# Kernel tuning notes

Hardware: AMD Instinct MI355X
Metric: run time of the kernel (lower is better)

The kernel has to match this reference:

```python
import jax, jax.numpy as jnp
import numpy as np

V = 50257  # vocab_size
H = 512    # d_model
S = 512    # source length
B = 8      # batch
T = 64     # decode steps


def setup_inputs() -> dict:
    key = jax.random.key(0)
    k1, k2, k3, k4, k5, k6 = jax.random.split(key, 6)
    src_full = jax.random.randint(k1, (S, B), 0, V, dtype=jnp.int32)
    decode_output = jax.random.normal(k2, (T, B, H), dtype=jnp.float32)
    decode_attn = jax.random.uniform(k3, (B, T, S), dtype=jnp.float32)
    memory = jax.random.normal(k4, (S, B, H), dtype=jnp.float32)
    # learned params: gen_proj (H->V) and prob_proj (H->1)
    W_gen = jax.random.normal(k5, (H, V), dtype=jnp.float32) / np.sqrt(H)
    b_gen = jnp.zeros((V,), dtype=jnp.float32)
    W_prob = jax.random.normal(k6, (H, 1), dtype=jnp.float32) / np.sqrt(H)
    b_prob = jnp.zeros((1,), dtype=jnp.float32)
    return {
        "src_full": src_full,
        "decode_output": decode_output,
        "decode_attn": decode_attn,
        "memory": memory,
        "W_gen": W_gen,
        "b_gen": b_gen,
        "W_prob": W_prob,
        "b_prob": b_prob,
    }


def reference(src_full, decode_output, decode_attn, memory, W_gen, b_gen, W_prob, b_prob):
    # context[t,b,h] = sum_s attn[b,t,s] * memory[s,b,h]
    context = jnp.einsum("bts,sbh->tbh", decode_attn, memory)  # [T,B,H]
    prob = jax.nn.sigmoid(context @ W_prob + b_prob)           # [T,B,1] copy gate p_gen
    gen_logits = prob * jax.nn.softmax(decode_output @ W_gen + b_gen, axis=-1)  # [T,B,V]

    # scatter-add attention mass onto vocab slots: copy[t,b, src_full[s,b]] += attn[b,t,s]
    attn_tbs = jnp.transpose(decode_attn, (1, 0, 2))  # [T,B,S]
    idx = src_full.T                                  # [B,S]
    ti = jnp.arange(T)[:, None, None]
    bi = jnp.arange(B)[None, :, None]
    copy_logits = jnp.zeros((T, B, V), dtype=decode_attn.dtype).at[ti, bi, idx[None, :, :]].add(attn_tbs)
    copy_logits = (1.0 - prob) * jax.nn.softmax(copy_logits, axis=-1)

    return jnp.log(gen_logits + copy_logits)
```

## Files before the change

### kernel.cpp

```cpp
#include <hip/hip_runtime.h>
#include <hip/hip_bf16.h>
#include <math.h>

#define VV 50257
#define VP 50304
#define HH 512
#define SS 512
#define BB 8
#define TT 64
#define MM (TT*BB)

typedef __bf16 bf16x2 __attribute__((ext_vector_type(2)));
typedef __bf16 bf16x4 __attribute__((ext_vector_type(4)));
typedef __bf16 bf16x8 __attribute__((ext_vector_type(8)));
typedef float  f32x4  __attribute__((ext_vector_type(4)));

__device__ __forceinline__ __bf16 f2b(float f) {
    unsigned u = __builtin_bit_cast(unsigned, f);
    unsigned r = (u + 0x7fffu + ((u >> 16) & 1u)) >> 16;
    unsigned short s = (unsigned short)r;
    return __builtin_bit_cast(__bf16, s);
}

__device__ __forceinline__ void gl2lds16(const void* g, void* l) {
    __builtin_amdgcn_global_load_lds(
        (const __attribute__((address_space(1))) unsigned*)g,
        (__attribute__((address_space(3))) unsigned*)l, 16, 0, 0);
}

__global__ __launch_bounds__(256) void k_castA(const float* __restrict__ A,
                                               __bf16* __restrict__ Ab) {
    int i = (blockIdx.x * 256 + threadIdx.x) * 4;
    float4 v = *(const float4*)&A[i];
    bf16x4 o = {f2b(v.x), f2b(v.y), f2b(v.z), f2b(v.w)};
    *(bf16x4*)&Ab[i] = o;
}

__global__ __launch_bounds__(256) void k_castWT(const float* __restrict__ W,
                                                __bf16* __restrict__ Wt) {
    __shared__ float tile[64][65];
    int n0 = blockIdx.x * 64;
    int k0 = blockIdx.y * 64;
    int tid = threadIdx.x;
#pragma unroll
    for (int i = 0; i < 16; i++) {
        int idx = tid + i * 256;
        int kk = idx >> 6, nn = idx & 63;
        int n = n0 + nn;
        tile[kk][nn] = (n < VV) ? W[(size_t)(k0 + kk) * VV + n] : 0.f;
    }
    __syncthreads();
#pragma unroll
    for (int i = 0; i < 8; i++) {
        int idx = tid + i * 256;
        int nn = idx >> 5, kp = idx & 31;
        bf16x2 o = {f2b(tile[2 * kp][nn]), f2b(tile[2 * kp + 1][nn])};
        *(bf16x2*)&Wt[(size_t)(n0 + nn) * HH + k0 + 2 * kp] = o;
    }
}

__global__ void k_mw(const float* __restrict__ mem, const float* __restrict__ Wp,
                     float* __restrict__ mw) {
    int row = blockIdx.x;
    int lane = threadIdx.x;
    const float* mp = mem + (size_t)row * HH;
    float acc = 0.f;
#pragma unroll
    for (int i = 0; i < HH / 64; i++)
        acc += mp[lane + 64 * i] * Wp[lane + 64 * i];
#pragma unroll
    for (int off = 32; off > 0; off >>= 1) acc += __shfl_down(acc, off);
    if (lane == 0) mw[row] = acc;
}

__global__ void k_prob(const float* __restrict__ attn, const float* __restrict__ mw,
                       const float* __restrict__ bp, float* __restrict__ prob) {
    int r = blockIdx.x;
    int t = r / BB, b = r % BB;
    int lane = threadIdx.x;
    const float* ap = attn + ((size_t)b * TT + t) * SS;
    float acc = 0.f;
#pragma unroll
    for (int i = 0; i < SS / 64; i++) {
        int s = lane + 64 * i;
        acc += ap[s] * mw[s * BB + b];
    }
#pragma unroll
    for (int off = 32; off > 0; off >>= 1) acc += __shfl_down(acc, off);
    if (lane == 0) prob[r] = 1.f / (1.f + expf(-(acc + bp[0])));
}

template<bool BF16OUT>
__global__ __launch_bounds__(512, 4) void k_gemm3(const __bf16* __restrict__ Ab,
                                                  const __bf16* __restrict__ Wt,
                                                  const float* __restrict__ bias,
                                                  float* __restrict__ Cf,
                                                  __bf16* __restrict__ Cb,
                                                  float* __restrict__ Zrow) {
    __shared__ __bf16 As[2][8192];
    __shared__ __bf16 Bs[2][8192];
    __shared__ float zred[128];

    const int tid  = threadIdx.x;
    const int lane = tid & 63;
    const int wave = tid >> 6;
    const int l15  = lane & 15;
    const int quad = lane >> 4;
    const int wr = (wave >> 2) * 64;
    const int wc = (wave & 3) * 32;

    int L = blockIdx.x + gridDim.x * blockIdx.y;
    int xcd = L & 7, i8 = L >> 3;
    int nid = (xcd < 4 ? xcd * 197 : 4 * 197 + (xcd - 4) * 196) + i8;
    const int row0 = (nid & 3) * 128;
    const int col0 = (nid >> 2) * 128;

    size_t offA[2], offB[2];
#pragma unroll
    for (int j = 0; j < 2; j++) {
        offA[j] = (size_t)(row0 + wave * 16 + l15) * HH + (j * 4 + quad) * 8;
        offB[j] = (size_t)(col0 + wave * 16 + l15) * HH + (j * 4 + quad) * 8;
    }

#define STAGE(buf, k0)                                                    \
    do {                                                                  \
        _Pragma("unroll") for (int j = 0; j < 2; j++) {                   \
            gl2lds16(Ab + offA[j] + (k0), &As[buf][wave * 1024 + j * 512]); \
            gl2lds16(Wt + offB[j] + (k0), &Bs[buf][wave * 1024 + j * 512]); \
        }                                                                 \
    } while (0)

    f32x4 acc[4][2] = {};

    STAGE(0, 0);
    for (int it = 0; it < 8; ++it) {
        __syncthreads();
        if (it != 7) STAGE((it + 1) & 1, (it + 1) * 64);
        const __bf16* Al = &As[it & 1][0];
        const __bf16* Bl = &Bs[it & 1][0];
#pragma unroll
        for (int h = 0; h < 2; ++h) {
            bf16x8 af[4], bfv[2];
#pragma unroll
            for (int mt = 0; mt < 4; mt++)
                af[mt] = *(const bf16x8*)&Al[((wr >> 4) + mt) * 1024 + h * 512 + lane * 8];
#pragma unroll
            for (int nt = 0; nt < 2; nt++)
                bfv[nt] = *(const bf16x8*)&Bl[((wc >> 4) + nt) * 1024 + h * 512 + lane * 8];
#pragma unroll
            for (int mt = 0; mt < 4; mt++)
#pragma unroll
                for (int nt = 0; nt < 2; nt++)
                    acc[mt][nt] = __builtin_amdgcn_mfma_f32_16x16x32_bf16(
                        af[mt], bfv[nt], acc[mt][nt], 0, 0, 0);
        }
    }
#undef STAGE

    __syncthreads();
    if (tid < 128) zred[tid] = 0.f;
    __syncthreads();

#pragma unroll
    for (int mt = 0; mt < 4; mt++) {
        float esum[4] = {0.f, 0.f, 0.f, 0.f};
#pragma unroll
        for (int nt = 0; nt < 2; nt++) {
            int c = col0 + wc + nt * 16 + l15;
            if (c < VV) {
                float bv = bias[c];
#pragma unroll
                for (int i = 0; i < 4; i++) {
                    int r = row0 + wr + mt * 16 + quad * 4 + i;
                    float l = acc[mt][nt][i] + bv;
                    if (BF16OUT) Cb[(size_t)r * VP + c] = f2b(l);
                    else         Cf[(size_t)r * VV + c] = l;
                    esum[i] += __expf(l);
                }
            }
        }
#pragma unroll
        for (int i = 0; i < 4; i++) {
            float e = esum[i];
            e += __shfl_xor(e, 1);
            e += __shfl_xor(e, 2);
            e += __shfl_xor(e, 4);
            e += __shfl_xor(e, 8);
            if (l15 == 0)
                atomicAdd(&zred[wr + mt * 16 + quad * 4 + i], e);
        }
    }
    __syncthreads();
    if (tid < 128) atomicAdd(&Zrow[row0 + tid], zred[tid]);
}

#define HT 1024
#define NBW 1572

__device__ __forceinline__ void build_hash(const int* __restrict__ src,
                                           const float* __restrict__ ap,
                                           int b, int tid,
                                           int* keys, float* vals, unsigned* bmap,
                                           float* red, int* s_D, float* s_Zc) {
    for (int i = tid; i < HT; i += 256) { keys[i] = -1; vals[i] = 0.f; }
    for (int i = tid; i < NBW; i += 256) bmap[i] = 0u;
    if (tid == 0) *s_D = 0;
    __syncthreads();

    for (int s = tid; s < SS; s += 256) {
        int idx = src[s * BB + b];
        float v = ap[s];
        unsigned h = ((unsigned)idx * 2654435761u) >> 22;
        while (true) {
            int old = atomicCAS(&keys[h], -1, idx);
            if (old == -1 || old == idx) { atomicAdd(&vals[h], v); break; }
            h = (h + 1) & (HT - 1);
        }
    }
    __syncthreads();

    float lsum = 0.f; int dloc = 0;
    for (int i = tid; i < HT; i += 256) {
        int k = keys[i];
        if (k != -1) {
            lsum += __expf(vals[i]); dloc++;
            atomicOr(&bmap[(unsigned)k >> 5], 1u << (k & 31));
        }
    }
    atomicAdd(s_D, dloc);
    red[tid] = lsum; __syncthreads();
    for (int st = 128; st > 0; st >>= 1) {
        if (tid < st) red[tid] += red[tid + st];
        __syncthreads();
    }
    if (tid == 0) *s_Zc = (float)(VV - *s_D) + red[0];
    __syncthreads();
}

__global__ __launch_bounds__(1024) void k_final_row(const int* __restrict__ src,
                                                    const float* __restrict__ attn,
                                                    const float* __restrict__ prob,
                                                    const float* __restrict__ Zrow,
                                                    const __bf16* __restrict__ LG,
                                                    float* __restrict__ out) {
    __shared__ int      keys[HT];
    __shared__ float    vals[HT];
    __shared__ unsigned bmap[NBW];
    __shared__ float    red[1024];
    __shared__ int      s_D;
    __shared__ float    s_Zc;

    int r = blockIdx.x;
    int t = r / BB, b = r % BB;
    int tid = threadIdx.x;
    const float* ap = attn + ((size_t)b * TT + t) * SS;

    { int i = tid; keys[i] = -1; vals[i] = 0.f; }
    for (int i = tid; i < NBW; i += 1024) bmap[i] = 0u;
    if (tid == 0) s_D = 0;
    __syncthreads();

    if (tid < SS) {
        int idx = src[tid * BB + b];
        float v = ap[tid];
        unsigned h = ((unsigned)idx * 2654435761u) >> 22;
        while (true) {
            int old = atomicCAS(&keys[h], -1, idx);
            if (old == -1 || old == idx) { atomicAdd(&vals[h], v); break; }
            h = (h + 1) & (HT - 1);
        }
    }
    __syncthreads();

    float lsum = 0.f;
    {
        int k = keys[tid];
        bool occ = (k != -1);
        if (occ) {
            lsum = __expf(vals[tid]);
            atomicOr(&bmap[(unsigned)k >> 5], 1u << (k & 31));
        }
        unsigned long long m = __ballot(occ);
        if ((tid & 63) == 0) atomicAdd(&s_D, __popcll(m));
    }
    red[tid] = lsum; __syncthreads();
    for (int st = 512; st > 0; st >>= 1) {
        if (tid < st) red[tid] += red[tid + st];
        __syncthreads();
    }
    if (tid == 0) s_Zc = (float)(VV - s_D) + red[0];
    __syncthreads();

    float p = prob[r];
    float pinvZ = p / Zrow[r];
    float qinvZc = (1.f - p) / s_Zc;

    const __bf16* lrow = LG + (size_t)r * VP;
    float* orow = out + (size_t)r * VV;

    for (int v0 = tid * 8; v0 < VP; v0 += 8192) {
        bf16x8 l8 = *(const bf16x8*)&lrow[v0];
#pragma unroll
        for (int e = 0; e < 8; e++) {
            int v = v0 + e;
            if (v < VV) {
                float l = (float)l8[e];
                float c = 1.f;
                if ((bmap[v >> 5] >> (v & 31)) & 1u) {
                    unsigned h = ((unsigned)v * 2654435761u) >> 22;
                    while (true) {
                        int k = keys[h];
                        if (k == v) { c = __expf(vals[h]); break; }
                        if (k == -1) break;
                        h = (h + 1) & (HT - 1);
                    }
                }
                orow[v] = __logf(pinvZ * __expf(l) + qinvZc * c);
            }
        }
    }
}

#define CHUNKS 6283
__global__ __launch_bounds__(256) void k_final_s(const int* __restrict__ src,
                                                 const float* __restrict__ attn,
                                                 const float* __restrict__ prob,
                                                 const float* __restrict__ Zrow,
                                                 float* __restrict__ out) {
    __shared__ int      keys[HT];
    __shared__ float    vals[HT];
    __shared__ unsigned bmap[NBW];
    __shared__ float    red[256];
    __shared__ int      s_D;
    __shared__ float    s_Zc;

    int r = blockIdx.y;
    int t = r / BB, b = r % BB;
    int tid = threadIdx.x;
    const float* ap = attn + ((size_t)b * TT + t) * SS;
    build_hash(src, ap, b, tid, keys, vals, bmap, red, &s_D, &s_Zc);

    float p = prob[r];
    float pinvZ = p / Zrow[r];
    float qinvZc = (1.f - p) / s_Zc;

    int c0 = blockIdx.x * CHUNKS;
    int c1 = c0 + CHUNKS; if (c1 > VV) c1 = VV;
    float* rowp = out + (size_t)r * VV;

    for (int v = c0 + tid; v < c1; v += 256) {
        float l = rowp[v];
        float c = 1.f;
        if ((bmap[v >> 5] >> (v & 31)) & 1u) {
            unsigned h = ((unsigned)v * 2654435761u) >> 22;
            while (true) {
                int k = keys[h];
                if (k == v) { c = __expf(vals[h]); break; }
                if (k == -1) break;
                h = (h + 1) & (HT - 1);
            }
        }
        rowp[v] = __logf(pinvZ * __expf(l) + qinvZc * c);
    }
}

extern "C" void kernel_launch(void* const* d_in, const int* in_sizes, int n_in,
                              void* d_out, int out_size, void* d_ws, size_t ws_size,
                              hipStream_t stream) {
    const int*   src_full      = (const int*)d_in[0];
    const float* decode_output = (const float*)d_in[1];
    const float* decode_attn   = (const float*)d_in[2];
    const float* memory        = (const float*)d_in[3];
    const float* W_gen         = (const float*)d_in[4];
    const float* b_gen         = (const float*)d_in[5];
    const float* W_prob        = (const float*)d_in[6];
    const float* b_prob        = (const float*)d_in[7];
    float* out = (float*)d_out;

    float* ws   = (float*)d_ws;
    float* mw   = ws;
    float* prob = ws + 4096;
    float* Z    = ws + 4608;
    __bf16* Ab  = (__bf16*)(ws + 5120);
    __bf16* Wt  = (__bf16*)(ws + 5120 + 131072);
    __bf16* LG  = Wt + (size_t)VP * HH;

    size_t base_b = (size_t)(5120 + 131072) * sizeof(float);
    size_t wt_b   = (size_t)VP * HH * 2;
    size_t lg_b   = (size_t)MM * VP * 2;
    bool full = ws_size >= base_b + wt_b + lg_b;

    k_castA<<<MM * HH / (256 * 4), 256, 0, stream>>>(decode_output, Ab);
    k_mw<<<SS * BB, 64, 0, stream>>>(memory, W_prob, mw);
    k_prob<<<TT * BB, 64, 0, stream>>>(decode_attn, mw, b_prob, prob);
    hipMemsetAsync(Z, 0, MM * sizeof(float), stream);

    dim3 tgrid(VP / 64, HH / 64);
    k_castWT<<<tgrid, 256, 0, stream>>>(W_gen, Wt);

    dim3 ggrid(MM / 128, VP / 128);
    if (full) {
        k_gemm3<true><<<ggrid, 512, 0, stream>>>(Ab, Wt, b_gen, nullptr, LG, Z);
        k_final_row<<<MM, 1024, 0, stream>>>(src_full, decode_attn, prob, Z, LG, out);
    } else {
        k_gemm3<false><<<ggrid, 512, 0, stream>>>(Ab, Wt, b_gen, out, nullptr, Z);
        dim3 fgrid((VV + CHUNKS - 1) / CHUNKS, MM);
        k_final_s<<<fgrid, 256, 0, stream>>>(src_full, decode_attn, prob, Z, out);
    }
}
```

Measured before the change: 364.8 us.

## Merge preprocessing launches and deepen GEMM LDS pipeline to four stages

The small preprocessing kernels (A cast, memory·W_prob dot, prob gate, Z memset, W transpose-cast) are merged into two combined launches, with Z zeroed inside the prob blocks instead of by a memset. The GEMM's K loop changes from double-buffered 64-wide steps to a four-buffer, 32-wide ring. Each step uses explicit vmcnt waits and a raw barrier, so up to three stages of global-to-LDS loads are in flight at once. This is meant to cut launch overhead and hide load latency, at the cost of more loop iterations and hand-managed wait counts that must match the issued loads exactly.

Result: faster. 355.3 us (-2.6%).

```diff
diff --git a/kernel.cpp b/kernel.cpp
--- a/kernel.cpp
+++ b/kernel.cpp
@@ -28,77 +28,90 @@
         (__attribute__((address_space(3))) unsigned*)l, 16, 0, 0);
 }
 
-__global__ __launch_bounds__(256) void k_castA(const float* __restrict__ A,
-                                               __bf16* __restrict__ Ab) {
-    int i = (blockIdx.x * 256 + threadIdx.x) * 4;
-    float4 v = *(const float4*)&A[i];
-    bf16x4 o = {f2b(v.x), f2b(v.y), f2b(v.z), f2b(v.w)};
-    *(bf16x4*)&Ab[i] = o;
-}
-
-__global__ __launch_bounds__(256) void k_castWT(const float* __restrict__ W,
-                                                __bf16* __restrict__ Wt) {
+#define WAITV(n) asm volatile("s_waitcnt vmcnt(" #n ")" ::: "memory")
+
+__global__ __launch_bounds__(256) void k_pre(const float* __restrict__ A,
+                                             __bf16* __restrict__ Ab,
+                                             const float* __restrict__ mem,
+                                             const float* __restrict__ Wp,
+                                             float* __restrict__ mw) {
+    int tid = threadIdx.x;
+    if (blockIdx.x < 256) {
+        int i = (blockIdx.x * 256 + tid) * 4;
+        float4 v = *(const float4*)&A[i];
+        bf16x4 o = {f2b(v.x), f2b(v.y), f2b(v.z), f2b(v.w)};
+        *(bf16x4*)&Ab[i] = o;
+    } else {
+        int bx = blockIdx.x - 256;
+        int row = bx * 4 + (tid >> 6);
+        int lane = tid & 63;
+        const float* mp = mem + (size_t)row * HH;
+        float acc = 0.f;
+#pragma unroll
+        for (int i = 0; i < HH / 64; i++)
+            acc += mp[lane + 64 * i] * Wp[lane + 64 * i];
+#pragma unroll
+        for (int off = 32; off > 0; off >>= 1) acc += __shfl_down(acc, off);
+        if (lane == 0) mw[row] = acc;
+    }
+}
+
+__global__ __launch_bounds__(256) void k_mid(const float* __restrict__ attn,
+                                             const float* __restrict__ mw,
+                                             const float* __restrict__ bp,
+                                             float* __restrict__ prob,
+                                             float* __restrict__ Z,
+                                             const float* __restrict__ W,
+                                             __bf16* __restrict__ Wt) {
     __shared__ float tile[64][65];
-    int n0 = blockIdx.x * 64;
-    int k0 = blockIdx.y * 64;
     int tid = threadIdx.x;
-#pragma unroll
-    for (int i = 0; i < 16; i++) {
-        int idx = tid + i * 256;
-        int kk = idx >> 6, nn = idx & 63;
-        int n = n0 + nn;
-        tile[kk][nn] = (n < VV) ? W[(size_t)(k0 + kk) * VV + n] : 0.f;
-    }
-    __syncthreads();
-#pragma unroll
-    for (int i = 0; i < 8; i++) {
-        int idx = tid + i * 256;
-        int nn = idx >> 5, kp = idx & 31;
-        bf16x2 o = {f2b(tile[2 * kp][nn]), f2b(tile[2 * kp + 1][nn])};
-        *(bf16x2*)&Wt[(size_t)(n0 + nn) * HH + k0 + 2 * kp] = o;
-    }
-}
-
-__global__ void k_mw(const float* __restrict__ mem, const float* __restrict__ Wp,
-                     float* __restrict__ mw) {
-    int row = blockIdx.x;
-    int lane = threadIdx.x;
-    const float* mp = mem + (size_t)row * HH;
-    float acc = 0.f;
-#pragma unroll
-    for (int i = 0; i < HH / 64; i++)
-        acc += mp[lane + 64 * i] * Wp[lane + 64 * i];
-#pragma unroll
-    for (int off = 32; off > 0; off >>= 1) acc += __shfl_down(acc, off);
-    if (lane == 0) mw[row] = acc;
-}
-
-__global__ void k_prob(const float* __restrict__ attn, const float* __restrict__ mw,
-                       const float* __restrict__ bp, float* __restrict__ prob) {
-    int r = blockIdx.x;
-    int t = r / BB, b = r % BB;
-    int lane = threadIdx.x;
-    const float* ap = attn + ((size_t)b * TT + t) * SS;
-    float acc = 0.f;
-#pragma unroll
-    for (int i = 0; i < SS / 64; i++) {
-        int s = lane + 64 * i;
-        acc += ap[s] * mw[s * BB + b];
-    }
-#pragma unroll
-    for (int off = 32; off > 0; off >>= 1) acc += __shfl_down(acc, off);
-    if (lane == 0) prob[r] = 1.f / (1.f + expf(-(acc + bp[0])));
+    if (blockIdx.x < 512) {
+        int r = blockIdx.x;
+        int t = r / BB, b = r % BB;
+        const float* ap = attn + ((size_t)b * TT + t) * SS;
+        float acc = ap[tid] * mw[tid * BB + b] +
+                    ap[tid + 256] * mw[(tid + 256) * BB + b];
+        float* red = &tile[0][0];
+        red[tid] = acc; __syncthreads();
+        for (int st = 128; st > 0; st >>= 1) {
+            if (tid < st) red[tid] += red[tid + st];
+            __syncthreads();
+        }
+        if (tid == 0) {
+            prob[r] = 1.f / (1.f + expf(-(red[0] + bp[0])));
+            Z[r] = 0.f;
+        }
+    } else {
+        int bx = blockIdx.x - 512;
+        int n0 = (bx % (VP / 64)) * 64;
+        int k0 = (bx / (VP / 64)) * 64;
+#pragma unroll
+        for (int i = 0; i < 16; i++) {
+            int idx = tid + i * 256;
+            int kk = idx >> 6, nn = idx & 63;
+            int n = n0 + nn;
+            tile[kk][nn] = (n < VV) ? W[(size_t)(k0 + kk) * VV + n] : 0.f;
+        }
+        __syncthreads();
+#pragma unroll
+        for (int i = 0; i < 8; i++) {
+            int idx = tid + i * 256;
+            int nn = idx >> 5, kp = idx & 31;
+            bf16x2 o = {f2b(tile[2 * kp][nn]), f2b(tile[2 * kp + 1][nn])};
+            *(bf16x2*)&Wt[(size_t)(n0 + nn) * HH + k0 + 2 * kp] = o;
+        }
+    }
 }
 
 template<bool BF16OUT>
-__global__ __launch_bounds__(512, 4) void k_gemm3(const __bf16* __restrict__ Ab,
+__global__ __launch_bounds__(512, 4) void k_gemm4(const __bf16* __restrict__ Ab,
                                                   const __bf16* __restrict__ Wt,
                                                   const float* __restrict__ bias,
                                                   float* __restrict__ Cf,
                                                   __bf16* __restrict__ Cb,
                                                   float* __restrict__ Zrow) {
-    __shared__ __bf16 As[2][8192];
-    __shared__ __bf16 Bs[2][8192];
+    __shared__ __bf16 As[4][4096];
+    __shared__ __bf16 Bs[4][4096];
     __shared__ float zred[128];
 
     const int tid  = threadIdx.x;
@@ -115,45 +128,42 @@
     const int row0 = (nid & 3) * 128;
     const int col0 = (nid >> 2) * 128;
 
-    size_t offA[2], offB[2];
-#pragma unroll
-    for (int j = 0; j < 2; j++) {
-        offA[j] = (size_t)(row0 + wave * 16 + l15) * HH + (j * 4 + quad) * 8;
-        offB[j] = (size_t)(col0 + wave * 16 + l15) * HH + (j * 4 + quad) * 8;
-    }
-
-#define STAGE(buf, k0)                                                    \
-    do {                                                                  \
-        _Pragma("unroll") for (int j = 0; j < 2; j++) {                   \
-            gl2lds16(Ab + offA[j] + (k0), &As[buf][wave * 1024 + j * 512]); \
-            gl2lds16(Wt + offB[j] + (k0), &Bs[buf][wave * 1024 + j * 512]); \
-        }                                                                 \
+    const size_t offA = (size_t)(row0 + wave * 16 + l15) * HH + quad * 8;
+    const size_t offB = (size_t)(col0 + wave * 16 + l15) * HH + quad * 8;
+
+#define STAGE(buf, k0)                                   \
+    do {                                                 \
+        gl2lds16(Ab + offA + (k0), &As[buf][wave * 512]); \
+        gl2lds16(Wt + offB + (k0), &Bs[buf][wave * 512]); \
     } while (0)
 
     f32x4 acc[4][2] = {};
 
     STAGE(0, 0);
-    for (int it = 0; it < 8; ++it) {
-        __syncthreads();
-        if (it != 7) STAGE((it + 1) & 1, (it + 1) * 64);
-        const __bf16* Al = &As[it & 1][0];
-        const __bf16* Bl = &Bs[it & 1][0];
-#pragma unroll
-        for (int h = 0; h < 2; ++h) {
-            bf16x8 af[4], bfv[2];
-#pragma unroll
-            for (int mt = 0; mt < 4; mt++)
-                af[mt] = *(const bf16x8*)&Al[((wr >> 4) + mt) * 1024 + h * 512 + lane * 8];
+    STAGE(1, 32);
+    STAGE(2, 64);
+#pragma unroll
+    for (int it = 0; it < 16; ++it) {
+        if (it <= 13)      WAITV(4);
+        else if (it == 14) WAITV(2);
+        else               WAITV(0);
+        __builtin_amdgcn_s_barrier();
+        if (it < 13) STAGE((it + 3) & 3, (it + 3) * 32);
+        const __bf16* Al = &As[it & 3][0];
+        const __bf16* Bl = &Bs[it & 3][0];
+        bf16x8 af[4], bfv[2];
+#pragma unroll
+        for (int mt = 0; mt < 4; mt++)
+            af[mt] = *(const bf16x8*)&Al[((wr >> 4) + mt) * 512 + lane * 8];
+#pragma unroll
+        for (int nt = 0; nt < 2; nt++)
+            bfv[nt] = *(const bf16x8*)&Bl[((wc >> 4) + nt) * 512 + lane * 8];
+#pragma unroll
+        for (int mt = 0; mt < 4; mt++)
 #pragma unroll
             for (int nt = 0; nt < 2; nt++)
-                bfv[nt] = *(const bf16x8*)&Bl[((wc >> 4) + nt) * 1024 + h * 512 + lane * 8];
-#pragma unroll
-            for (int mt = 0; mt < 4; mt++)
-#pragma unroll
-                for (int nt = 0; nt < 2; nt++)
-                    acc[mt][nt] = __builtin_amdgcn_mfma_f32_16x16x32_bf16(
-                        af[mt], bfv[nt], acc[mt][nt], 0, 0, 0);
-        }
+                acc[mt][nt] = __builtin_amdgcn_mfma_f32_16x16x32_bf16(
+                    af[mt], bfv[nt], acc[mt][nt], 0, 0, 0);
     }
 #undef STAGE
 
@@ -390,20 +400,16 @@
     size_t lg_b   = (size_t)MM * VP * 2;
     bool full = ws_size >= base_b + wt_b + lg_b;
 
-    k_castA<<<MM * HH / (256 * 4), 256, 0, stream>>>(decode_output, Ab);
-    k_mw<<<SS * BB, 64, 0, stream>>>(memory, W_prob, mw);
-    k_prob<<<TT * BB, 64, 0, stream>>>(decode_attn, mw, b_prob, prob);
-    hipMemsetAsync(Z, 0, MM * sizeof(float), stream);
-
-    dim3 tgrid(VP / 64, HH / 64);
-    k_castWT<<<tgrid, 256, 0, stream>>>(W_gen, Wt);
+    k_pre<<<1280, 256, 0, stream>>>(decode_output, Ab, memory, W_prob, mw);
+    k_mid<<<512 + (VP / 64) * (HH / 64), 256, 0, stream>>>(
+        decode_attn, mw, b_prob, prob, Z, W_gen, Wt);
 
     dim3 ggrid(MM / 128, VP / 128);
     if (full) {
-        k_gemm3<true><<<ggrid, 512, 0, stream>>>(Ab, Wt, b_gen, nullptr, LG, Z);
+        k_gemm4<true><<<ggrid, 512, 0, stream>>>(Ab, Wt, b_gen, nullptr, LG, Z);
         k_final_row<<<MM, 1024, 0, stream>>>(src_full, decode_attn, prob, Z, LG, out);
     } else {
-        k_gemm3<false><<<ggrid, 512, 0, stream>>>(Ab, Wt, b_gen, out, nullptr, Z);
+        k_gemm4<false><<<ggrid, 512, 0, stream>>>(Ab, Wt, b_gen, out, nullptr, Z);
         dim3 fgrid((VV + CHUNKS - 1) / CHUNKS, MM);
         k_final_s<<<fgrid, 256, 0, stream>>>(src_full, decode_attn, prob, Z, out);
     }
```
